# Performance work log

Hardware: AMD Instinct MI355X
Metric: run time of the kernel (lower is better)

The kernel has to match this reference:

```python
import jax, jax.numpy as jnp
import numpy as np

N_NODES = 50000
NEG_SLOPE = 0.2


def _gat_layer(x, src, dst, W, att_src, att_dst, bias, concat):
    # x: [N, F_in]; W: [F_in, H*D]; att_*: [H, D]; bias: [H*D] or [D]
    H, D = att_src.shape
    N = x.shape[0]
    h = (x @ W).reshape(N, H, D)                       # [N, H, D]
    a_s = jnp.einsum('nhd,hd->nh', h, att_src)         # [N, H]
    a_d = jnp.einsum('nhd,hd->nh', h, att_dst)
    e = a_s[src] + a_d[dst]                            # [E, H]
    e = jnp.where(e > 0, e, NEG_SLOPE * e)             # LeakyReLU(0.2)
    # segment softmax over incoming edges of each target node
    e_max = jax.ops.segment_max(e, dst, num_segments=N)
    ex = jnp.exp(e - e_max[dst])
    denom = jax.ops.segment_sum(ex, dst, num_segments=N)
    alpha = ex / denom[dst]                            # [E, H]
    msg = h[src] * alpha[:, :, None]                   # [E, H, D]
    out = jax.ops.segment_sum(msg, dst, num_segments=N)  # [N, H, D]
    if concat:
        out = out.reshape(N, H * D)
    else:
        out = out.mean(axis=1)
    return out + bias


def _forward(x, edge_index, W1, att_src1, att_dst1, b1, W2, att_src2, att_dst2, b2):
    N = x.shape[0]
    loop = jnp.arange(N, dtype=edge_index.dtype)
    src = jnp.concatenate([edge_index[0], loop])       # add self-loops (PyG default)
    dst = jnp.concatenate([edge_index[1], loop])
    h = _gat_layer(x, src, dst, W1, att_src1, att_dst1, b1, concat=True)
    h = jax.nn.elu(h)
    h = _gat_layer(h, src, dst, W2, att_src2, att_dst2, b2, concat=False)
    return jax.nn.log_softmax(h, axis=-1)


def setup_inputs() -> dict:
    key = jax.random.key(0)
    ks = jax.random.split(key, 12)
    N, E, F_in, F_out, H, D = N_NODES, 1600000, 128, 64, 8, 32
    glorot = lambda k, shp: jax.random.normal(k, shp, jnp.float32) * np.sqrt(2.0 / (shp[0] + shp[-1]))
    return {
        'x': jax.random.normal(ks[0], (N, F_in), jnp.float32),
        'edge_index': jax.random.randint(ks[1], (2, E), 0, N, jnp.int64),
        'W1': glorot(ks[2], (F_in, H * D)),
        'att_src1': glorot(ks[3], (H, D)),
        'att_dst1': glorot(ks[4], (H, D)),
        'b1': jnp.zeros((H * D,), jnp.float32),
        'W2': glorot(ks[5], (H * D, F_out)),
        'att_src2': glorot(ks[6], (1, F_out)),
        'att_dst2': glorot(ks[7], (1, F_out)),
        'b2': jnp.zeros((F_out,), jnp.float32),
    }


def reference(x, edge_index, W1, att_src1, att_dst1, b1, W2, att_src2, att_dst2, b2):
    return _forward(x, edge_index, W1, att_src1, att_dst1, b1, W2, att_src2, att_dst2, b2)
```

## Files before the change

### kernel.cpp

```cpp
#include <hip/hip_runtime.h>
#include <hip/hip_bf16.h>
#include <math.h>


#define FIN 128
#define C1 256
#define NH 8
#define HD 32
#define C2 64
#define CH1 64

typedef float floatx2 __attribute__((ext_vector_type(2)));
typedef short bf16x8 __attribute__((ext_vector_type(8)));
typedef float f32x4 __attribute__((ext_vector_type(4)));

__device__ __forceinline__ float blo(unsigned u) { return __uint_as_float(u << 16); }
__device__ __forceinline__ float bhi(unsigned u) { return __uint_as_float(u & 0xffff0000u); }
__device__ __forceinline__ unsigned pkbf(float a, float b) {
    unsigned ua = __float_as_uint(a), ub = __float_as_uint(b);
    ua += 0x7fff + ((ua >> 16) & 1);
    ub += 0x7fff + ((ub >> 16) & 1);
    return (ua >> 16) | (ub & 0xffff0000u);
}

__global__ void zero_kernel(int* p, int n) {
    int i = blockIdx.x * 256 + threadIdx.x;
    if (i < n) p[i] = 0;
}

__global__ void hist_kernel(const int* __restrict__ ei, int E, int ETOT, int T,
                            int* cnt, int* __restrict__ offs) {
    int base = blockIdx.x * 256 + threadIdx.x;
    if (base >= T) return;
    int d[8], o[8];
    #pragma unroll
    for (int i = 0; i < 8; ++i) {
        int e = base + i * T;
        d[i] = (e < ETOT) ? ((e < E) ? ei[E + e] : (e - E)) : -1;
    }
    #pragma unroll
    for (int i = 0; i < 8; ++i)
        if (d[i] >= 0) o[i] = atomicAdd(&cnt[d[i]], 1);
    #pragma unroll
    for (int i = 0; i < 8; ++i)
        if (d[i] >= 0) offs[base + i * T] = o[i];
}

__global__ void scan1_kernel(const int* __restrict__ cnt, int n,
                             int* __restrict__ pref, int* __restrict__ bsum) {
    int tid = threadIdx.x, lane = tid & 63, w = tid >> 6;
    int i = blockIdx.x * 256 + tid;
    int v = (i < n) ? cnt[i] : 0;
    int sc = v;
    #pragma unroll
    for (int d = 1; d < 64; d <<= 1) {
        int t = __shfl_up(sc, d, 64);
        if (lane >= d) sc += t;
    }
    __shared__ int ws[4];
    if (lane == 63) ws[w] = sc;
    __syncthreads();
    int woff = 0;
    #pragma unroll
    for (int k = 0; k < 4; ++k) woff += (k < w) ? ws[k] : 0;
    if (i < n) pref[i] = woff + sc - v;
    if (tid == 255) bsum[blockIdx.x] = woff + sc;
}

__global__ void scan2_kernel(int* bsum, int nb) {
    int tid = threadIdx.x, lane = tid & 63, w = tid >> 6;
    int v = (tid < nb) ? bsum[tid] : 0;
    int sc = v;
    #pragma unroll
    for (int d = 1; d < 64; d <<= 1) {
        int t = __shfl_up(sc, d, 64);
        if (lane >= d) sc += t;
    }
    __shared__ int ws[4];
    if (lane == 63) ws[w] = sc;
    __syncthreads();
    int woff = 0;
    #pragma unroll
    for (int k = 0; k < 4; ++k) woff += (k < w) ? ws[k] : 0;
    __syncthreads();
    if (tid < nb) bsum[tid] = woff + sc - v;
}

__global__ void scan3_kernel(const int* __restrict__ pref, const int* __restrict__ bsum,
                             int n, int ETOT, int* __restrict__ rowptr) {
    int i = blockIdx.x * 256 + threadIdx.x;
    if (i < n) rowptr[i] = pref[i] + bsum[blockIdx.x];
    if (i == 0) rowptr[n] = ETOT;
}

__global__ void scatter_kernel(const int* __restrict__ ei, const int* __restrict__ rowptr,
                               const int* __restrict__ offs, int E, int ETOT, int T,
                               int* __restrict__ colb) {
    int base = blockIdx.x * 256 + threadIdx.x;
    if (base >= T) return;
    #pragma unroll
    for (int i = 0; i < 8; ++i) {
        int e = base + i * T;
        if (e >= ETOT) continue;
        int src, dst;
        if (e < E) { src = ei[e]; dst = ei[E + e]; }
        else       { src = e - E; dst = e - E; }
        colb[rowptr[dst] + offs[e]] = src;
    }
}

__global__ void cvt_x_kernel(const float* __restrict__ x, unsigned* __restrict__ xb, int total8) {
    int i = blockIdx.x * 256 + threadIdx.x;
    if (i >= total8) return;
    const float4* p = reinterpret_cast<const float4*>(x + (size_t)i * 8);
    float4 v0 = p[0], v1 = p[1];
    uint4 o;
    o.x = pkbf(v0.x, v0.y); o.y = pkbf(v0.z, v0.w);
    o.z = pkbf(v1.x, v1.y); o.w = pkbf(v1.z, v1.w);
    reinterpret_cast<uint4*>(xb)[i] = o;
}

__global__ void cvt_w1_kernel(const float* __restrict__ W1, unsigned short* __restrict__ w1t) {
    int k = blockIdx.x, j = threadIdx.x;
    float v = W1[k * C1 + j];
    w1t[j * FIN + k] = (unsigned short)(pkbf(v, v) & 0xffffu);
}

__global__ void cvt_w2_kernel(const float* __restrict__ W2, unsigned short* __restrict__ w2t) {
    int j = blockIdx.x, k = threadIdx.x;
    float v = W2[k * C2 + j];
    w2t[j * C1 + k] = (unsigned short)(pkbf(v, v) & 0xffffu);
}

__global__ __launch_bounds__(256) void gemm1_mfma(
    const unsigned short* __restrict__ xb, const unsigned short* __restrict__ w1t,
    unsigned char* __restrict__ h1, int Nn) {
    __shared__ __align__(16) unsigned char sA[64 * 256];
    int tid = threadIdx.x;
    int row0 = blockIdx.x * 64;
    #pragma unroll
    for (int rep = 0; rep < 4; ++rep) {
        int flat = rep * 256 + tid;
        int row = flat >> 4, c16 = flat & 15;
        uint4 v = make_uint4(0u, 0u, 0u, 0u);
        if (row0 + row < Nn)
            v = *reinterpret_cast<const uint4*>(
                reinterpret_cast<const unsigned char*>(xb) + (size_t)(row0 + row) * 256 + c16 * 16);
        *reinterpret_cast<uint4*>(sA + ((row * 256 + c16 * 16) ^ ((row & 7) << 4))) = v;
    }
    __syncthreads();
    int w = tid >> 6, l = tid & 63;
    int lr = l & 15, lq = l >> 4;
    int arow = w * 16 + lr;
    bf16x8 a[4];
    #pragma unroll
    for (int ks = 0; ks < 4; ++ks)
        a[ks] = *reinterpret_cast<const bf16x8*>(
            sA + ((arow * 256 + ks * 64 + lq * 16) ^ ((arow & 7) << 4)));
    const unsigned char* wb = reinterpret_cast<const unsigned char*>(w1t);
    #pragma unroll
    for (int nt = 0; nt < 16; ++nt) {
        f32x4 acc = {0.f, 0.f, 0.f, 0.f};
        #pragma unroll
        for (int ks = 0; ks < 4; ++ks) {
            bf16x8 b = *reinterpret_cast<const bf16x8*>(
                wb + (size_t)(nt * 16 + lr) * 256 + ks * 64 + lq * 16);
            acc = __builtin_amdgcn_mfma_f32_16x16x32_bf16(a[ks], b, acc, 0, 0, 0);
        }
        int col = nt * 16 + lr;
        #pragma unroll
        for (int reg = 0; reg < 4; ++reg) {
            int row = row0 + w * 16 + lq * 4 + reg;
            if (row < Nn) {
                unsigned pk = __builtin_amdgcn_cvt_pk_fp8_f32(acc[reg], acc[reg], 0, false);
                h1[(size_t)row * C1 + col] = (unsigned char)(pk & 0xffu);
            }
        }
    }
}

__global__ __launch_bounds__(256) void att1_kernel(
    const unsigned char* __restrict__ h1, const float* __restrict__ att_s,
    const float* __restrict__ att_d, float* __restrict__ as1, float* __restrict__ ad1, int Nn) {
    int tid = threadIdx.x;
    int row = blockIdx.x * 16 + (tid >> 4);
    int l16 = tid & 15;
    if (row >= Nn) return;
    uint4 u = *reinterpret_cast<const uint4*>(h1 + (size_t)row * C1 + l16 * 16);
    float hv[16];
    unsigned uu[4] = {u.x, u.y, u.z, u.w};
    #pragma unroll
    for (int q = 0; q < 4; ++q) {
        floatx2 f0 = __builtin_amdgcn_cvt_pk_f32_fp8((int)uu[q], false);
        floatx2 f1 = __builtin_amdgcn_cvt_pk_f32_fp8((int)uu[q], true);
        hv[q * 4 + 0] = f0.x; hv[q * 4 + 1] = f0.y;
        hv[q * 4 + 2] = f1.x; hv[q * 4 + 3] = f1.y;
    }
    int col0 = l16 * 16;
    const float4* asp = reinterpret_cast<const float4*>(att_s + col0);
    const float4* adp = reinterpret_cast<const float4*>(att_d + col0);
    float ps = 0.f, pd = 0.f;
    #pragma unroll
    for (int q = 0; q < 4; ++q) {
        float4 sa = asp[q], da = adp[q];
        ps += hv[q*4+0]*sa.x + hv[q*4+1]*sa.y + hv[q*4+2]*sa.z + hv[q*4+3]*sa.w;
        pd += hv[q*4+0]*da.x + hv[q*4+1]*da.y + hv[q*4+2]*da.z + hv[q*4+3]*da.w;
    }
    ps += __shfl_xor(ps, 1, 64);
    pd += __shfl_xor(pd, 1, 64);
    if ((l16 & 1) == 0) {
        as1[row * NH + (l16 >> 1)] = ps;
        ad1[row * NH + (l16 >> 1)] = pd;
    }
}

__global__ __launch_bounds__(256) void agg1_kernel(
    const int* __restrict__ rowptr, const int* __restrict__ colb,
    const float* __restrict__ as1, const float* __restrict__ ad1,
    const unsigned char* __restrict__ h1, const float* __restrict__ b1,
    __hip_bfloat16* __restrict__ x1e, int N) {
    int wid = threadIdx.x >> 6, lane = threadIdx.x & 63;
    int n = blockIdx.x * 4 + wid;
    __shared__ float sp[4][CH1 * 9];
    __shared__ int ssrc[4][CH1];
    __shared__ float advs[4][NH];
    if (n >= N) return;
    int start = rowptr[n], end = rowptr[n + 1];
    int h = lane >> 3, sub = lane & 7;
    int half = lane >> 5, l5 = lane & 31;
    int hq = l5 >> 2;
    ssrc[wid][lane] = 0;
    if (lane < NH) advs[wid][lane] = ad1[n * NH + lane];
    float adr[NH];
    #pragma unroll
    for (int hh = 0; hh < NH; ++hh) adr[hh] = advs[wid][hh];

    float m = -INFINITY, denom = 0.f;
    floatx2 A01 = {0.f, 0.f}, A23 = {0.f, 0.f}, A45 = {0.f, 0.f}, A67 = {0.f, 0.f};
    for (int base = start; base < end; base += CH1) {
        int cn = min(CH1, end - base);
        if (lane < cn) {
            int s = colb[base + lane];
            ssrc[wid][lane] = s;
            const float4* ap = reinterpret_cast<const float4*>(as1 + (size_t)s * NH);
            float4 q0 = ap[0], q1 = ap[1];
            float av[8] = {q0.x, q0.y, q0.z, q0.w, q1.x, q1.y, q1.z, q1.w};
            #pragma unroll
            for (int hh = 0; hh < NH; ++hh) {
                float e = av[hh] + adr[hh];
                e = e > 0.f ? e : 0.2f * e;
                sp[wid][lane * 9 + hh] = e;
            }
        }
        float cmax = -INFINITY;
        for (int e = sub; e < cn; e += 8) cmax = fmaxf(cmax, sp[wid][e * 9 + h]);
        #pragma unroll
        for (int mk = 4; mk >= 1; mk >>= 1) cmax = fmaxf(cmax, __shfl_xor(cmax, mk, 64));
        float newm = fmaxf(m, cmax);
        float scale = __expf(m - newm);
        float scale_g = __shfl(scale, hq << 3, 64);
        floatx2 s2 = {scale_g, scale_g};
        A01 *= s2; A23 *= s2; A45 *= s2; A67 *= s2;
        denom *= scale; m = newm;
        float psum = 0.f;
        for (int e = sub; e < cn; e += 8) {
            float p = __expf(sp[wid][e * 9 + h] - m);
            sp[wid][e * 9 + h] = p;
            psum += p;
        }
        #pragma unroll
        for (int mk = 4; mk >= 1; mk >>= 1) psum += __shfl_xor(psum, mk, 64);
        denom += psum;
        #pragma unroll 2
        for (int e2 = 0; e2 < cn; e2 += 2) {
            int e = e2 + half;
            bool ok = e < cn;
            int s = ssrc[wid][ok ? e : 0];
            float p = ok ? sp[wid][e * 9 + hq] : 0.f;
            floatx2 p2 = {p, p};
            uint2 u = *reinterpret_cast<const uint2*>(h1 + (size_t)s * C1 + l5 * 8);
            floatx2 f01 = __builtin_amdgcn_cvt_pk_f32_fp8((int)u.x, false);
            floatx2 f23 = __builtin_amdgcn_cvt_pk_f32_fp8((int)u.x, true);
            floatx2 f45 = __builtin_amdgcn_cvt_pk_f32_fp8((int)u.y, false);
            floatx2 f67 = __builtin_amdgcn_cvt_pk_f32_fp8((int)u.y, true);
            A01 = __builtin_elementwise_fma(p2, f01, A01);
            A23 = __builtin_elementwise_fma(p2, f23, A23);
            A45 = __builtin_elementwise_fma(p2, f45, A45);
            A67 = __builtin_elementwise_fma(p2, f67, A67);
        }
    }
    float a0 = A01.x, a1 = A01.y, a2 = A23.x, a3 = A23.y;
    float a4 = A45.x, a5 = A45.y, a6 = A67.x, a7 = A67.y;
    a0 += __shfl_xor(a0, 32, 64); a1 += __shfl_xor(a1, 32, 64);
    a2 += __shfl_xor(a2, 32, 64); a3 += __shfl_xor(a3, 32, 64);
    a4 += __shfl_xor(a4, 32, 64); a5 += __shfl_xor(a5, 32, 64);
    a6 += __shfl_xor(a6, 32, 64); a7 += __shfl_xor(a7, 32, 64);
    float invd = 1.f / __shfl(denom, hq << 3, 64);
    if (half == 0) {
        const float4* bp = reinterpret_cast<const float4*>(b1 + l5 * 8);
        float4 bv0 = bp[0], bv1 = bp[1];
        float v0 = a0 * invd + bv0.x, v1 = a1 * invd + bv0.y;
        float v2 = a2 * invd + bv0.z, v3 = a3 * invd + bv0.w;
        float v4 = a4 * invd + bv1.x, v5 = a5 * invd + bv1.y;
        float v6 = a6 * invd + bv1.z, v7 = a7 * invd + bv1.w;
        v0 = v0 > 0.f ? v0 : __expf(v0) - 1.f;
        v1 = v1 > 0.f ? v1 : __expf(v1) - 1.f;
        v2 = v2 > 0.f ? v2 : __expf(v2) - 1.f;
        v3 = v3 > 0.f ? v3 : __expf(v3) - 1.f;
        v4 = v4 > 0.f ? v4 : __expf(v4) - 1.f;
        v5 = v5 > 0.f ? v5 : __expf(v5) - 1.f;
        v6 = v6 > 0.f ? v6 : __expf(v6) - 1.f;
        v7 = v7 > 0.f ? v7 : __expf(v7) - 1.f;
        uint4 w;
        w.x = pkbf(v0, v1); w.y = pkbf(v2, v3);
        w.z = pkbf(v4, v5); w.w = pkbf(v6, v7);
        *reinterpret_cast<uint4*>(x1e + (size_t)n * C1 + l5 * 8) = w;
    }
}

__global__ __launch_bounds__(256) void gemm2_mfma(
    const unsigned short* __restrict__ x1e, const unsigned short* __restrict__ w2t,
    unsigned short* __restrict__ h2, int Nn) {
    __shared__ __align__(16) unsigned char sA[64 * 512];
    int tid = threadIdx.x;
    int row0 = blockIdx.x * 64;
    #pragma unroll
    for (int rep = 0; rep < 8; ++rep) {
        int flat = rep * 256 + tid;
        int row = flat >> 5, c16 = flat & 31;
        uint4 v = make_uint4(0u, 0u, 0u, 0u);
        if (row0 + row < Nn)
            v = *reinterpret_cast<const uint4*>(
                reinterpret_cast<const unsigned char*>(x1e) + (size_t)(row0 + row) * 512 + c16 * 16);
        *reinterpret_cast<uint4*>(sA + ((row * 512 + c16 * 16) ^ ((row & 7) << 4))) = v;
    }
    __syncthreads();
    int w = tid >> 6, l = tid & 63;
    int lr = l & 15, lq = l >> 4;
    int arow = w * 16 + lr;
    bf16x8 a[8];
    #pragma unroll
    for (int ks = 0; ks < 8; ++ks)
        a[ks] = *reinterpret_cast<const bf16x8*>(
            sA + ((arow * 512 + ks * 64 + lq * 16) ^ ((arow & 7) << 4)));
    const unsigned char* wb = reinterpret_cast<const unsigned char*>(w2t);
    #pragma unroll
    for (int nt = 0; nt < 4; ++nt) {
        f32x4 acc = {0.f, 0.f, 0.f, 0.f};
        #pragma unroll
        for (int ks = 0; ks < 8; ++ks) {
            bf16x8 b = *reinterpret_cast<const bf16x8*>(
                wb + (size_t)(nt * 16 + lr) * 512 + ks * 64 + lq * 16);
            acc = __builtin_amdgcn_mfma_f32_16x16x32_bf16(a[ks], b, acc, 0, 0, 0);
        }
        int col = nt * 16 + lr;
        #pragma unroll
        for (int reg = 0; reg < 4; ++reg) {
            int row = row0 + w * 16 + lq * 4 + reg;
            if (row < Nn)
                h2[(size_t)row * C2 + col] = (unsigned short)(pkbf(acc[reg], acc[reg]) & 0xffffu);
        }
    }
}

__global__ __launch_bounds__(256) void att2_kernel(
    const unsigned short* __restrict__ h2, const float* __restrict__ att_s2,
    const float* __restrict__ att_d2, float* __restrict__ as2, float* __restrict__ ad2, int Nn) {
    int tid = threadIdx.x;
    int row = blockIdx.x * 16 + (tid >> 4);
    int l16 = tid & 15;
    if (row >= Nn) return;
    uint2 u = *reinterpret_cast<const uint2*>(h2 + (size_t)row * C2 + l16 * 4);
    float h0 = blo(u.x), h1v = bhi(u.x), h2v = blo(u.y), h3 = bhi(u.y);
    const float4* asp = reinterpret_cast<const float4*>(att_s2 + l16 * 4);
    const float4* adp = reinterpret_cast<const float4*>(att_d2 + l16 * 4);
    float4 sa = asp[0], da = adp[0];
    float ps = h0*sa.x + h1v*sa.y + h2v*sa.z + h3*sa.w;
    float pd = h0*da.x + h1v*da.y + h2v*da.z + h3*da.w;
    #pragma unroll
    for (int mk = 8; mk >= 1; mk >>= 1) {
        ps += __shfl_xor(ps, mk, 64);
        pd += __shfl_xor(pd, mk, 64);
    }
    if (l16 == 0) { as2[row] = ps; ad2[row] = pd; }
}

__global__ __launch_bounds__(256) void agg2_kernel(
    const int* __restrict__ rowptr, const int* __restrict__ colb,
    const float* __restrict__ as2, const float* __restrict__ ad2,
    const __hip_bfloat16* __restrict__ h2, const float* __restrict__ b2,
    float* __restrict__ out, int N) {
    int wid = threadIdx.x >> 6, lane = threadIdx.x & 63;
    int n = blockIdx.x * 4 + wid;
    __shared__ float sp2[4][64];
    __shared__ int ssrc2[4][64];
    if (n >= N) return;
    int start = rowptr[n], end = rowptr[n + 1];
    int q = lane >> 4, l4 = lane & 15;
    ssrc2[wid][lane] = 0;
    float adn = ad2[n];
    float m = -INFINITY, denom = 0.f;
    floatx2 A01 = {0.f, 0.f}, A23 = {0.f, 0.f};
    for (int base = start; base < end; base += 64) {
        int cn = min(64, end - base);
        float logit = -INFINITY;
        if (lane < cn) {
            int s = colb[base + lane];
            ssrc2[wid][lane] = s;
            float e = as2[s] + adn;
            logit = e > 0.f ? e : 0.2f * e;
        }
        float cmax = logit;
        #pragma unroll
        for (int mk = 32; mk >= 1; mk >>= 1) cmax = fmaxf(cmax, __shfl_xor(cmax, mk, 64));
        float newm = fmaxf(m, cmax);
        float scale = __expf(m - newm);
        floatx2 s2 = {scale, scale};
        A01 *= s2; A23 *= s2;
        denom *= scale; m = newm;
        float p = (lane < cn) ? __expf(logit - m) : 0.f;
        sp2[wid][lane] = p;
        float psum = p;
        #pragma unroll
        for (int mk = 32; mk >= 1; mk >>= 1) psum += __shfl_xor(psum, mk, 64);
        denom += psum;
        #pragma unroll 2
        for (int e2 = 0; e2 < cn; e2 += 4) {
            int e = e2 + q;
            bool ok = e < cn;
            int s = ssrc2[wid][ok ? e : 0];
            float pe = ok ? sp2[wid][e] : 0.f;
            floatx2 p2 = {pe, pe};
            uint2 u = *reinterpret_cast<const uint2*>(h2 + (size_t)s * C2 + l4 * 4);
            floatx2 f01 = {blo(u.x), bhi(u.x)};
            floatx2 f23 = {blo(u.y), bhi(u.y)};
            A01 = __builtin_elementwise_fma(p2, f01, A01);
            A23 = __builtin_elementwise_fma(p2, f23, A23);
        }
    }
    float a0 = A01.x, a1 = A01.y, a2 = A23.x, a3 = A23.y;
    a0 += __shfl_xor(a0, 16, 64); a1 += __shfl_xor(a1, 16, 64);
    a2 += __shfl_xor(a2, 16, 64); a3 += __shfl_xor(a3, 16, 64);
    a0 += __shfl_xor(a0, 32, 64); a1 += __shfl_xor(a1, 32, 64);
    a2 += __shfl_xor(a2, 32, 64); a3 += __shfl_xor(a3, 32, 64);
    float invd = 1.f / denom;
    const float4* bp = reinterpret_cast<const float4*>(b2 + l4 * 4);
    float4 bv = bp[0];
    float v0 = a0 * invd + bv.x, v1 = a1 * invd + bv.y;
    float v2 = a2 * invd + bv.z, v3 = a3 * invd + bv.w;
    float mx = fmaxf(fmaxf(v0, v1), fmaxf(v2, v3));
    #pragma unroll
    for (int mk = 8; mk >= 1; mk >>= 1) mx = fmaxf(mx, __shfl_xor(mx, mk, 64));
    float sum = __expf(v0 - mx) + __expf(v1 - mx) + __expf(v2 - mx) + __expf(v3 - mx);
    #pragma unroll
    for (int mk = 8; mk >= 1; mk >>= 1) sum += __shfl_xor(sum, mk, 64);
    float ls = logf(sum);
    if (q == 0) {
        float4 o = make_float4(v0 - mx - ls, v1 - mx - ls, v2 - mx - ls, v3 - mx - ls);
        *reinterpret_cast<float4*>(out + (size_t)n * C2 + l4 * 4) = o;
    }
}

extern "C" void kernel_launch(void* const* d_in, const int* in_sizes, int n_in,
                              void* d_out, int out_size, void* d_ws, size_t ws_size,
                              hipStream_t stream) {
    const float* x      = (const float*)d_in[0];
    const int*   ei     = (const int*)d_in[1];
    const float* W1     = (const float*)d_in[2];
    const float* att_s1 = (const float*)d_in[3];
    const float* att_d1 = (const float*)d_in[4];
    const float* b1     = (const float*)d_in[5];
    const float* W2     = (const float*)d_in[6];
    const float* att_s2 = (const float*)d_in[7];
    const float* att_d2 = (const float*)d_in[8];
    const float* b2     = (const float*)d_in[9];
    float* out = (float*)d_out;

    const int N = out_size / C2;
    const int E = in_sizes[1] / 2;
    const int ETOT = E + N;
    const int NB = (N + 255) / 256;

    char* ws = (char*)d_ws;
    size_t off = 0;
    auto alloc = [&](size_t bytes) -> void* {
        void* p = ws + off;
        off += (bytes + 255) & ~(size_t)255;
        return p;
    };
    unsigned char* h1 = (unsigned char*)alloc((size_t)N * C1);
    __hip_bfloat16* x1e = (__hip_bfloat16*)alloc((size_t)N * C1 * 2);
    unsigned* xb = (unsigned*)alloc((size_t)N * FIN * 2);
    unsigned short* w1t = (unsigned short*)alloc((size_t)C1 * FIN * 2);
    unsigned short* w2t = (unsigned short*)alloc((size_t)C2 * C1 * 2);
    float* as1  = (float*)alloc((size_t)N * NH * 4);
    float* ad1  = (float*)alloc((size_t)N * NH * 4);
    float* as2  = (float*)alloc((size_t)N * 4);
    float* ad2  = (float*)alloc((size_t)N * 4);
    int*   cnt    = (int*)alloc((size_t)N * 4);
    int*   rowptr = (int*)alloc((size_t)(N + 1) * 4);
    int*   pref   = (int*)alloc((size_t)N * 4);
    int*   bsum   = (int*)alloc((size_t)NB * 4);
    int*   offs   = (int*)alloc((size_t)ETOT * 4);
    int*   colb   = (int*)alloc((size_t)ETOT * 4);
    unsigned short* h2 = (unsigned short*)h1;

    const int T = (ETOT + 7) / 8;
    zero_kernel<<<(N + 255) / 256, 256, 0, stream>>>(cnt, N);
    hist_kernel<<<(T + 255) / 256, 256, 0, stream>>>(ei, E, ETOT, T, cnt, offs);
    scan1_kernel<<<NB, 256, 0, stream>>>(cnt, N, pref, bsum);
    scan2_kernel<<<1, 256, 0, stream>>>(bsum, NB);
    scan3_kernel<<<NB, 256, 0, stream>>>(pref, bsum, N, ETOT, rowptr);
    scatter_kernel<<<(T + 255) / 256, 256, 0, stream>>>(ei, rowptr, offs, E, ETOT, T, colb);

    int total8 = N * FIN / 8;
    cvt_x_kernel<<<(total8 + 255) / 256, 256, 0, stream>>>(x, xb, total8);
    cvt_w1_kernel<<<FIN, C1, 0, stream>>>(W1, w1t);
    cvt_w2_kernel<<<C2, C1, 0, stream>>>(W2, w2t);

    gemm1_mfma<<<(N + 63) / 64, 256, 0, stream>>>((const unsigned short*)xb, w1t, h1, N);
    att1_kernel<<<(N + 15) / 16, 256, 0, stream>>>(h1, att_s1, att_d1, as1, ad1, N);
    agg1_kernel<<<(N + 3) / 4, 256, 0, stream>>>(rowptr, colb, as1, ad1, h1, b1, x1e, N);

    gemm2_mfma<<<(N + 63) / 64, 256, 0, stream>>>((const unsigned short*)x1e, w2t, h2, N);
    att2_kernel<<<(N + 15) / 16, 256, 0, stream>>>(h2, att_s2, att_d2, as2, ad2, N);
    agg2_kernel<<<(N + 3) / 4, 256, 0, stream>>>(rowptr, colb, as2, ad2,
                                                 (const __hip_bfloat16*)h2, b2, out, N);
}
```

Baseline: 301.8 us.

## Widen agg1 gathers to 16-byte loads, precompute byte offsets, halve edges per thread

The layer-1 aggregation now has each lane load 16 fp8 features (uint4) instead of 8, and processes four edges per wave-iteration instead of two. This means fewer, wider gather instructions, at the cost of more accumulator registers and a wider cross-lane reduction. Source indices are stored in shared memory as precomputed byte offsets (s<<8, s<<7) in both aggregation kernels, which removes the 64-bit multiply-add per gather. The hist and scatter kernels now handle 4 edges per thread instead of 8, which doubles the thread count.

```diff
diff --git a/kernel.cpp b/kernel.cpp
--- a/kernel.cpp
+++ b/kernel.cpp
@@ -32,17 +32,17 @@
                             int* cnt, int* __restrict__ offs) {
     int base = blockIdx.x * 256 + threadIdx.x;
     if (base >= T) return;
-    int d[8], o[8];
-    #pragma unroll
-    for (int i = 0; i < 8; ++i) {
+    int d[4], o[4];
+    #pragma unroll
+    for (int i = 0; i < 4; ++i) {
         int e = base + i * T;
         d[i] = (e < ETOT) ? ((e < E) ? ei[E + e] : (e - E)) : -1;
     }
     #pragma unroll
-    for (int i = 0; i < 8; ++i)
+    for (int i = 0; i < 4; ++i)
         if (d[i] >= 0) o[i] = atomicAdd(&cnt[d[i]], 1);
     #pragma unroll
-    for (int i = 0; i < 8; ++i)
+    for (int i = 0; i < 4; ++i)
         if (d[i] >= 0) offs[base + i * T] = o[i];
 }
 
@@ -99,7 +99,7 @@
     int base = blockIdx.x * 256 + threadIdx.x;
     if (base >= T) return;
     #pragma unroll
-    for (int i = 0; i < 8; ++i) {
+    for (int i = 0; i < 4; ++i) {
         int e = base + i * T;
         if (e >= ETOT) continue;
         int src, dst;
@@ -222,29 +222,32 @@
     int wid = threadIdx.x >> 6, lane = threadIdx.x & 63;
     int n = blockIdx.x * 4 + wid;
     __shared__ float sp[4][CH1 * 9];
-    __shared__ int ssrc[4][CH1];
+    __shared__ int soff[4][CH1];
     __shared__ float advs[4][NH];
     if (n >= N) return;
     int start = rowptr[n], end = rowptr[n + 1];
     int h = lane >> 3, sub = lane & 7;
-    int half = lane >> 5, l5 = lane & 31;
-    int hq = l5 >> 2;
-    ssrc[wid][lane] = 0;
+    int q4 = lane >> 4, l4 = lane & 15;
+    int hq = l4 >> 1;
+    soff[wid][lane] = 0;
     if (lane < NH) advs[wid][lane] = ad1[n * NH + lane];
     float adr[NH];
     #pragma unroll
     for (int hh = 0; hh < NH; ++hh) adr[hh] = advs[wid][hh];
 
     float m = -INFINITY, denom = 0.f;
-    floatx2 A01 = {0.f, 0.f}, A23 = {0.f, 0.f}, A45 = {0.f, 0.f}, A67 = {0.f, 0.f};
+    floatx2 A[8];
+    #pragma unroll
+    for (int i = 0; i < 8; ++i) A[i] = (floatx2){0.f, 0.f};
+
     for (int base = start; base < end; base += CH1) {
         int cn = min(CH1, end - base);
         if (lane < cn) {
             int s = colb[base + lane];
-            ssrc[wid][lane] = s;
+            soff[wid][lane] = s << 8;
             const float4* ap = reinterpret_cast<const float4*>(as1 + (size_t)s * NH);
-            float4 q0 = ap[0], q1 = ap[1];
-            float av[8] = {q0.x, q0.y, q0.z, q0.w, q1.x, q1.y, q1.z, q1.w};
+            float4 qq0 = ap[0], qq1 = ap[1];
+            float av[8] = {qq0.x, qq0.y, qq0.z, qq0.w, qq1.x, qq1.y, qq1.z, qq1.w};
             #pragma unroll
             for (int hh = 0; hh < NH; ++hh) {
                 float e = av[hh] + adr[hh];
@@ -260,7 +263,8 @@
         float scale = __expf(m - newm);
         float scale_g = __shfl(scale, hq << 3, 64);
         floatx2 s2 = {scale_g, scale_g};
-        A01 *= s2; A23 *= s2; A45 *= s2; A67 *= s2;
+        #pragma unroll
+        for (int i = 0; i < 8; ++i) A[i] *= s2;
         denom *= scale; m = newm;
         float psum = 0.f;
         for (int e = sub; e < cn; e += 8) {
@@ -272,49 +276,61 @@
         for (int mk = 4; mk >= 1; mk >>= 1) psum += __shfl_xor(psum, mk, 64);
         denom += psum;
         #pragma unroll 2
-        for (int e2 = 0; e2 < cn; e2 += 2) {
-            int e = e2 + half;
+        for (int e4 = 0; e4 < cn; e4 += 4) {
+            int e = e4 + q4;
             bool ok = e < cn;
-            int s = ssrc[wid][ok ? e : 0];
+            int off = soff[wid][ok ? e : 0];
             float p = ok ? sp[wid][e * 9 + hq] : 0.f;
             floatx2 p2 = {p, p};
-            uint2 u = *reinterpret_cast<const uint2*>(h1 + (size_t)s * C1 + l5 * 8);
-            floatx2 f01 = __builtin_amdgcn_cvt_pk_f32_fp8((int)u.x, false);
-            floatx2 f23 = __builtin_amdgcn_cvt_pk_f32_fp8((int)u.x, true);
-            floatx2 f45 = __builtin_amdgcn_cvt_pk_f32_fp8((int)u.y, false);
-            floatx2 f67 = __builtin_amdgcn_cvt_pk_f32_fp8((int)u.y, true);
-            A01 = __builtin_elementwise_fma(p2, f01, A01);
-            A23 = __builtin_elementwise_fma(p2, f23, A23);
-            A45 = __builtin_elementwise_fma(p2, f45, A45);
-            A67 = __builtin_elementwise_fma(p2, f67, A67);
-        }
-    }
-    float a0 = A01.x, a1 = A01.y, a2 = A23.x, a3 = A23.y;
-    float a4 = A45.x, a5 = A45.y, a6 = A67.x, a7 = A67.y;
-    a0 += __shfl_xor(a0, 32, 64); a1 += __shfl_xor(a1, 32, 64);
-    a2 += __shfl_xor(a2, 32, 64); a3 += __shfl_xor(a3, 32, 64);
-    a4 += __shfl_xor(a4, 32, 64); a5 += __shfl_xor(a5, 32, 64);
-    a6 += __shfl_xor(a6, 32, 64); a7 += __shfl_xor(a7, 32, 64);
+            uint4 u = *reinterpret_cast<const uint4*>(h1 + off + l4 * 16);
+            floatx2 f0 = __builtin_amdgcn_cvt_pk_f32_fp8((int)u.x, false);
+            floatx2 f1 = __builtin_amdgcn_cvt_pk_f32_fp8((int)u.x, true);
+            floatx2 f2 = __builtin_amdgcn_cvt_pk_f32_fp8((int)u.y, false);
+            floatx2 f3 = __builtin_amdgcn_cvt_pk_f32_fp8((int)u.y, true);
+            floatx2 f4 = __builtin_amdgcn_cvt_pk_f32_fp8((int)u.z, false);
+            floatx2 f5 = __builtin_amdgcn_cvt_pk_f32_fp8((int)u.z, true);
+            floatx2 f6 = __builtin_amdgcn_cvt_pk_f32_fp8((int)u.w, false);
+            floatx2 f7 = __builtin_amdgcn_cvt_pk_f32_fp8((int)u.w, true);
+            A[0] = __builtin_elementwise_fma(p2, f0, A[0]);
+            A[1] = __builtin_elementwise_fma(p2, f1, A[1]);
+            A[2] = __builtin_elementwise_fma(p2, f2, A[2]);
+            A[3] = __builtin_elementwise_fma(p2, f3, A[3]);
+            A[4] = __builtin_elementwise_fma(p2, f4, A[4]);
+            A[5] = __builtin_elementwise_fma(p2, f5, A[5]);
+            A[6] = __builtin_elementwise_fma(p2, f6, A[6]);
+            A[7] = __builtin_elementwise_fma(p2, f7, A[7]);
+        }
+    }
+    #pragma unroll
+    for (int i = 0; i < 8; ++i) {
+        A[i].x += __shfl_xor(A[i].x, 16, 64);
+        A[i].y += __shfl_xor(A[i].y, 16, 64);
+        A[i].x += __shfl_xor(A[i].x, 32, 64);
+        A[i].y += __shfl_xor(A[i].y, 32, 64);
+    }
     float invd = 1.f / __shfl(denom, hq << 3, 64);
-    if (half == 0) {
-        const float4* bp = reinterpret_cast<const float4*>(b1 + l5 * 8);
-        float4 bv0 = bp[0], bv1 = bp[1];
-        float v0 = a0 * invd + bv0.x, v1 = a1 * invd + bv0.y;
-        float v2 = a2 * invd + bv0.z, v3 = a3 * invd + bv0.w;
-        float v4 = a4 * invd + bv1.x, v5 = a5 * invd + bv1.y;
-        float v6 = a6 * invd + bv1.z, v7 = a7 * invd + bv1.w;
-        v0 = v0 > 0.f ? v0 : __expf(v0) - 1.f;
-        v1 = v1 > 0.f ? v1 : __expf(v1) - 1.f;
-        v2 = v2 > 0.f ? v2 : __expf(v2) - 1.f;
-        v3 = v3 > 0.f ? v3 : __expf(v3) - 1.f;
-        v4 = v4 > 0.f ? v4 : __expf(v4) - 1.f;
-        v5 = v5 > 0.f ? v5 : __expf(v5) - 1.f;
-        v6 = v6 > 0.f ? v6 : __expf(v6) - 1.f;
-        v7 = v7 > 0.f ? v7 : __expf(v7) - 1.f;
-        uint4 w;
-        w.x = pkbf(v0, v1); w.y = pkbf(v2, v3);
-        w.z = pkbf(v4, v5); w.w = pkbf(v6, v7);
-        *reinterpret_cast<uint4*>(x1e + (size_t)n * C1 + l5 * 8) = w;
+    if (q4 == 0) {
+        float v[16];
+        #pragma unroll
+        for (int i = 0; i < 8; ++i) { v[2*i] = A[i].x; v[2*i+1] = A[i].y; }
+        const float4* bp = reinterpret_cast<const float4*>(b1 + l4 * 16);
+        #pragma unroll
+        for (int qb = 0; qb < 4; ++qb) {
+            float4 bv = bp[qb];
+            v[qb*4+0] = v[qb*4+0] * invd + bv.x;
+            v[qb*4+1] = v[qb*4+1] * invd + bv.y;
+            v[qb*4+2] = v[qb*4+2] * invd + bv.z;
+            v[qb*4+3] = v[qb*4+3] * invd + bv.w;
+        }
+        #pragma unroll
+        for (int i = 0; i < 16; ++i) v[i] = v[i] > 0.f ? v[i] : __expf(v[i]) - 1.f;
+        uint4 w0, w1;
+        w0.x = pkbf(v[0], v[1]);  w0.y = pkbf(v[2], v[3]);
+        w0.z = pkbf(v[4], v[5]);  w0.w = pkbf(v[6], v[7]);
+        w1.x = pkbf(v[8], v[9]);  w1.y = pkbf(v[10], v[11]);
+        w1.z = pkbf(v[12], v[13]); w1.w = pkbf(v[14], v[15]);
+        uint4* op = reinterpret_cast<uint4*>(x1e + (size_t)n * C1 + l4 * 16);
+        op[0] = w0; op[1] = w1;
     }
 }
 
@@ -393,11 +409,11 @@
     int wid = threadIdx.x >> 6, lane = threadIdx.x & 63;
     int n = blockIdx.x * 4 + wid;
     __shared__ float sp2[4][64];
-    __shared__ int ssrc2[4][64];
+    __shared__ int soff2[4][64];
     if (n >= N) return;
     int start = rowptr[n], end = rowptr[n + 1];
     int q = lane >> 4, l4 = lane & 15;
-    ssrc2[wid][lane] = 0;
+    soff2[wid][lane] = 0;
     float adn = ad2[n];
     float m = -INFINITY, denom = 0.f;
     floatx2 A01 = {0.f, 0.f}, A23 = {0.f, 0.f};
@@ -406,7 +422,7 @@
         float logit = -INFINITY;
         if (lane < cn) {
             int s = colb[base + lane];
-            ssrc2[wid][lane] = s;
+            soff2[wid][lane] = s << 7;
             float e = as2[s] + adn;
             logit = e > 0.f ? e : 0.2f * e;
         }
@@ -428,10 +444,11 @@
         for (int e2 = 0; e2 < cn; e2 += 4) {
             int e = e2 + q;
             bool ok = e < cn;
-            int s = ssrc2[wid][ok ? e : 0];
+            int off = soff2[wid][ok ? e : 0];
             float pe = ok ? sp2[wid][e] : 0.f;
             floatx2 p2 = {pe, pe};
-            uint2 u = *reinterpret_cast<const uint2*>(h2 + (size_t)s * C2 + l4 * 4);
+            uint2 u = *reinterpret_cast<const uint2*>(
+                reinterpret_cast<const unsigned char*>(h2) + off + l4 * 8);
             floatx2 f01 = {blo(u.x), bhi(u.x)};
             floatx2 f23 = {blo(u.y), bhi(u.y)};
             A01 = __builtin_elementwise_fma(p2, f01, A01);
@@ -505,7 +522,7 @@
     int*   colb   = (int*)alloc((size_t)ETOT * 4);
     unsigned short* h2 = (unsigned short*)h1;
 
-    const int T = (ETOT + 7) / 8;
+    const int T = (ETOT + 3) / 4;
     zero_kernel<<<(N + 255) / 256, 256, 0, stream>>>(cnt, N);
     hist_kernel<<<(T + 255) / 256, 256, 0, stream>>>(ei, E, ETOT, T, cnt, offs);
     scan1_kernel<<<NB, 256, 0, stream>>>(cnt, N, pref, bsum);
```

Measured after the change: 303.3 us. Within noise of the previous version (+0.5%).
